# Optimization experiments

Measured on AMD Instinct MI355X. Metric: run time of the kernel, lower is better.

## Reference

```python
import jax, jax.numpy as jnp
import numpy as np

ZERO_EXP = -128.0  # exponent assigned to (near-)zero values, matching torch int8 fill


def _exp_quant_dequant(t):
    """Round-trip through the ExpFloat format.

    exponent = clamp(round(log2(|t|)), -128, 127) for |t| > 1e-38 else -128.
    Dequant is pow(2, exponent) -- note the sign is DISCARDED (faithful to
    ExpFloat.to_tensor, which never applies the stored sign), so the result
    is always positive.
    """
    a = jnp.abs(t)
    mask = a > 1e-38
    # guard log2 input with 1.0 where masked to avoid -inf/nan
    e = jnp.clip(jnp.round(jnp.log2(jnp.where(mask, a, 1.0))), -128.0, 127.0)
    e = jnp.where(mask, e, ZERO_EXP)
    return jnp.exp2(e)


def setup_inputs() -> dict:
    key = jax.random.key(0)
    k1, k2, k3 = jax.random.split(key, 3)
    N, IN, OUT = 8192, 4096, 4096
    x = jax.random.normal(k1, (N, IN), dtype=jnp.float32)
    # kaiming-uniform-ish scale for weight, uniform bias bound 1/sqrt(fan_in)
    bound_w = float(np.sqrt(6.0 / ((1.0 + 5.0) * IN)))
    weight = jax.random.uniform(k2, (OUT, IN), dtype=jnp.float32,
                                minval=-bound_w, maxval=bound_w)
    bound_b = 1.0 / float(np.sqrt(IN))
    bias = jax.random.uniform(k3, (OUT,), dtype=jnp.float32,
                              minval=-bound_b, maxval=bound_b)
    return {"x": x, "weight": weight, "bias": bias}


def reference(x, weight, bias):
    # quantized forward path of ExpFloatLinear (after .quantize()):
    # 1) x and W.T are quantized to power-of-two magnitudes (sign dropped)
    xq = _exp_quant_dequant(x)             # [N, IN]
    wq = _exp_quant_dequant(weight.T)      # [IN, OUT]
    # 2) dense matmul in dequantized domain
    m = jnp.matmul(xq, wq)                 # [N, OUT]
    # 3) matmul result re-quantized (ExpFloat.matmul returns ExpFloat(result))
    mq = _exp_quant_dequant(m)
    # 4) bias dequantized, added, and the sum quantized once more before to_tensor
    bq = _exp_quant_dequant(bias)          # [OUT]
    out = _exp_quant_dequant(mq + bq)      # [N, OUT]
    return out
```

## Files before the change

### kernel.cpp

```cpp
#include <hip/hip_runtime.h>
#include <hip/hip_bf16.h>
#include <stdint.h>

typedef __attribute__((ext_vector_type(8))) short short8;
typedef __attribute__((ext_vector_type(4))) float f32x4;

#define M_ROWS 8192
#define K_DIM  4096
#define N_COLS 4096
#define NT     (K_DIM / 64)
#define NWG    ((M_ROWS / 256) * (N_COLS / 256))
#define WL_CAP (1 << 20)

#define SQRT2_MANT 0x6A09E667F3BCDLL
#define FLAG_MARGIN 3110000000000LL

__device__ __forceinline__ int rlog2_mask(double a) {
    if (!(a > 1e-38)) return -128;
    long long b = __double_as_longlong(a);
    int E = (int)(b >> 52) - 1023;
    long long m = b & 0xFFFFFFFFFFFFFLL;
    int e = E + (int)(m >= SQRT2_MANT);
    return e < -128 ? -128 : (e > 127 ? 127 : e);
}

__device__ __forceinline__ double pow2d(int e) {
    return __longlong_as_double((long long)(e + 1023) << 52);
}

__device__ __forceinline__ unsigned short bf16_pow2(int e) {
    if (e >= -126) return (unsigned short)((e + 127) << 7);
    int sh = 133 + e;
    return (unsigned short)(sh >= 0 ? (1 << sh) : 0);
}

__device__ __forceinline__ int bf16_exp(unsigned short u) {
    int ex = (u >> 7) & 0xFF;
    if (ex) return ex - 127;
    int m = u & 0x7F;
    return m ? (-133 + (31 - __clz(m))) : -1000;
}

__device__ __forceinline__ float finalize_out(int em, int ebj) {
    double s = pow2d(em) + pow2d(ebj);
    return (float)pow2d(rlog2_mask(s));
}

__global__ void quant_kernel(const float* __restrict__ in, unsigned short* __restrict__ outq, int n4) {
    int idx = blockIdx.x * blockDim.x + threadIdx.x;
    int stride = gridDim.x * blockDim.x;
    for (int i = idx; i < n4; i += stride) {
        float4 v = ((const float4*)in)[i];
        ushort4 o;
        o.x = bf16_pow2(rlog2_mask(fabs((double)v.x)));
        o.y = bf16_pow2(rlog2_mask(fabs((double)v.y)));
        o.z = bf16_pow2(rlog2_mask(fabs((double)v.z)));
        o.w = bf16_pow2(rlog2_mask(fabs((double)v.w)));
        ((ushort4*)outq)[i] = o;
    }
}

__global__ void quant_bias_kernel(const float* __restrict__ b, int* __restrict__ eb, int n) {
    int i = blockIdx.x * blockDim.x + threadIdx.x;
    if (i < n) eb[i] = rlog2_mask(fabs((double)b[i]));
}

__device__ __forceinline__ void g2lds16(const unsigned short* g, unsigned short* l) {
    __builtin_amdgcn_global_load_lds(
        (const __attribute__((address_space(1))) unsigned int*)g,
        (__attribute__((address_space(3))) unsigned int*)l, 16, 0, 0);
}

#define LD8(p, off) (*(const short8*)((const char*)(p) + (off)))
#define MFMA16(a, b, c) __builtin_amdgcn_mfma_f32_16x16x32_bf16((a), (b), (c), 0, 0, 0)

__global__ __launch_bounds__(512, 2) void gemm_kernel(
    const unsigned short* __restrict__ xq, const unsigned short* __restrict__ wq,
    const int* __restrict__ eb, float* __restrict__ out,
    int* __restrict__ wl_count, int* __restrict__ wl)
{
    __shared__ unsigned short lds[2][32768];

    const int tid = threadIdx.x;
    const int lane = tid & 63, w = tid >> 6;
    const int wm = w >> 2, wn = w & 3;
    const int l15 = lane & 15, lhi = lane >> 4;

    const int x = blockIdx.x & 7;
    const int j = blockIdx.x >> 3;
    const int bm = (x & 3) * 8 + (j & 7);
    const int bn = (x >> 2) * 8 + ((j >> 3) & 3) + (j >> 5) * 4;
    const int brow = bm * 256, bcol = bn * 256;

    int p0 = tid * 16;
    int lin0 = p0 ^ (((p0 >> 9) & 1) << 5);
    int row0 = (lin0 >> 6) & 127;
    int col0 = (((lin0 >> 13) << 6) | (lin0 & 63)) >> 1;
    int p1 = 8192 + tid * 16;
    int lin1 = p1 ^ (((p1 >> 9) & 1) << 5);
    int row1 = (lin1 >> 6) & 127;
    int col1 = (((lin1 >> 13) << 6) | (lin1 & 63)) >> 1;

    const unsigned short* aS0h0 = xq + (size_t)(brow + row0) * K_DIM + col0;
    const unsigned short* aS1h0 = xq + (size_t)(brow + row1) * K_DIM + col1;
    const unsigned short* aS0h1 = aS0h0 + (size_t)128 * K_DIM;
    const unsigned short* aS1h1 = aS1h0 + (size_t)128 * K_DIM;
    const unsigned short* bS0h0 = wq + (size_t)(bcol + row0) * K_DIM + col0;
    const unsigned short* bS1h0 = wq + (size_t)(bcol + row1) * K_DIM + col1;
    const unsigned short* bS0h1 = bS0h0 + (size_t)128 * K_DIM;
    const unsigned short* bS1h1 = bS1h0 + (size_t)128 * K_DIM;

    const int wofs = w * 512;

#define STAGE_A(b, h, OFFE) do { \
        g2lds16(((h) ? aS0h1 : aS0h0) + (OFFE), &lds[b][(h) * 8192] + wofs); \
        g2lds16(((h) ? aS1h1 : aS1h0) + (OFFE), &lds[b][(h) * 8192 + 4096] + wofs); \
    } while (0)
#define STAGE_B(b, h, OFFE) do { \
        g2lds16(((h) ? bS0h1 : bS0h0) + (OFFE), &lds[b][16384 + (h) * 8192] + wofs); \
        g2lds16(((h) ? bS1h1 : bS1h0) + (OFFE), &lds[b][16384 + (h) * 8192 + 4096] + wofs); \
    } while (0)

    int fsw = l15 * 64 + lhi * 16;
    fsw ^= ((l15 >> 3) & 1) << 5;

    const char* pA_0 = (const char*)&lds[0][wm * 8192] + fsw;
    const char* pA_1 = (const char*)&lds[1][wm * 8192] + fsw;
    const char* pB_0 = (const char*)&lds[0][16384 + (wn >> 1) * 8192 + (wn & 1) * 2048] + fsw;
    const char* pB_1 = (const char*)&lds[1][16384 + (wn >> 1) * 8192 + (wn & 1) * 2048] + fsw;

    f32x4 acc[8][4];
#pragma unroll
    for (int m = 0; m < 8; ++m)
#pragma unroll
        for (int n = 0; n < 4; ++n) acc[m][n] = (f32x4){0.f, 0.f, 0.f, 0.f};

    short8 aF[4][2], b01[2][2], b23[2][2];

#define DS_A4(P, mb) do { \
        aF[0][0] = LD8(P, ((mb) + 0) * 1024); aF[0][1] = LD8(P, ((mb) + 0) * 1024 + 8192); \
        aF[1][0] = LD8(P, ((mb) + 1) * 1024); aF[1][1] = LD8(P, ((mb) + 1) * 1024 + 8192); \
        aF[2][0] = LD8(P, ((mb) + 2) * 1024); aF[2][1] = LD8(P, ((mb) + 2) * 1024 + 8192); \
        aF[3][0] = LD8(P, ((mb) + 3) * 1024); aF[3][1] = LD8(P, ((mb) + 3) * 1024 + 8192); \
    } while (0)
#define DS_B2(P, arr, cb) do { \
        arr[0][0] = LD8(P, ((cb) + 0) * 1024); arr[0][1] = LD8(P, ((cb) + 0) * 1024 + 8192); \
        arr[1][0] = LD8(P, ((cb) + 1) * 1024); arr[1][1] = LD8(P, ((cb) + 1) * 1024 + 8192); \
    } while (0)
#define MFMA_Q(mb, nb, B) do { \
        _Pragma("unroll") \
        for (int m_ = 0; m_ < 4; ++m_) \
        _Pragma("unroll") \
        for (int n_ = 0; n_ < 2; ++n_) { \
            acc[(mb) + m_][(nb) + n_] = MFMA16(aF[m_][0], B[n_][0], acc[(mb) + m_][(nb) + n_]); \
            acc[(mb) + m_][(nb) + n_] = MFMA16(aF[m_][1], B[n_][1], acc[(mb) + m_][(nb) + n_]); \
        } \
    } while (0)

#define BAR()  __builtin_amdgcn_s_barrier()
#define PRIO1() __builtin_amdgcn_s_setprio(1)
#define PRIO0() __builtin_amdgcn_s_setprio(0)

    STAGE_A(0, 0, 0);
    STAGE_A(0, 1, 0);
    STAGE_B(0, 0, 0);
    STAGE_B(0, 1, 0);
    STAGE_B(1, 0, 64);
    STAGE_B(1, 1, 64);
    asm volatile("s_waitcnt vmcnt(4)" ::: "memory");
    BAR();

    for (int tt = 0; tt < NT / 2 - 1; ++tt) {
        DS_B2(pB_0, b01, 0); DS_B2(pB_0, b23, 2);
        DS_A4(pA_0, 0);
        STAGE_A(1, 0, 64); STAGE_A(1, 1, 64);
        PRIO1(); MFMA_Q(0, 0, b01); MFMA_Q(0, 2, b23); PRIO0(); BAR();
        DS_A4(pA_0, 4);
        STAGE_B(0, 0, 128); STAGE_B(0, 1, 128);
        PRIO1(); MFMA_Q(4, 2, b23); MFMA_Q(4, 0, b01); PRIO0();
        asm volatile("s_waitcnt vmcnt(4)" ::: "memory");
        BAR();
        DS_B2(pB_1, b01, 0); DS_B2(pB_1, b23, 2);
        DS_A4(pA_1, 0);
        STAGE_A(0, 0, 128); STAGE_A(0, 1, 128);
        PRIO1(); MFMA_Q(0, 0, b01); MFMA_Q(0, 2, b23); PRIO0(); BAR();
        DS_A4(pA_1, 4);
        STAGE_B(1, 0, 192); STAGE_B(1, 1, 192);
        PRIO1(); MFMA_Q(4, 2, b23); MFMA_Q(4, 0, b01); PRIO0();
        asm volatile("s_waitcnt vmcnt(4)" ::: "memory");
        BAR();

        aS0h0 += 128; aS1h0 += 128; aS0h1 += 128; aS1h1 += 128;
        bS0h0 += 128; bS1h0 += 128; bS0h1 += 128; bS1h1 += 128;
    }

    DS_B2(pB_0, b01, 0); DS_B2(pB_0, b23, 2);
    DS_A4(pA_0, 0);
    STAGE_A(1, 0, 64); STAGE_A(1, 1, 64);
    PRIO1(); MFMA_Q(0, 0, b01); MFMA_Q(0, 2, b23); PRIO0(); BAR();
    DS_A4(pA_0, 4);
    PRIO1(); MFMA_Q(4, 2, b23); MFMA_Q(4, 0, b01); PRIO0();
    asm volatile("s_waitcnt vmcnt(0)" ::: "memory");
    BAR();
    DS_B2(pB_1, b01, 0); DS_B2(pB_1, b23, 2);
    DS_A4(pA_1, 0);
    PRIO1(); MFMA_Q(0, 0, b01); MFMA_Q(0, 2, b23); PRIO0(); BAR();
    DS_A4(pA_1, 4);
    PRIO1(); MFMA_Q(4, 2, b23); MFMA_Q(4, 0, b01); PRIO0();

#pragma unroll
    for (int m = 0; m < 8; ++m) {
        int grow_base = brow + wm * 128 + m * 16 + lhi * 4;
#pragma unroll
        for (int n = 0; n < 4; ++n) {
            int gcol = bcol + wn * 64 + n * 16 + l15;
            int ebj = eb[gcol];
#pragma unroll
            for (int q = 0; q < 4; ++q) {
                float S = acc[m][n][q];
                int grow = grow_base + q;
                double v = (double)S;
                int em; bool flag;
                if (v > 1e-38) {
                    long long bb = __double_as_longlong(v);
                    long long mm = bb & 0xFFFFFFFFFFFFFLL;
                    long long d = mm - SQRT2_MANT;
                    flag = (d < 0 ? -d : d) < FLAG_MARGIN;
                    int e = ((int)(bb >> 52) - 1023) + (int)(mm >= SQRT2_MANT);
                    em = e < -128 ? -128 : (e > 127 ? 127 : e);
                } else { em = -128; flag = true; }
                out[(size_t)grow * N_COLS + gcol] = finalize_out(em, ebj);
                if (flag) {
                    int pos = atomicAdd(wl_count, 1);
                    if (pos < WL_CAP) wl[pos] = grow * N_COLS + gcol;
                }
            }
        }
    }
}

__global__ __launch_bounds__(256) void fixup_kernel(
    const unsigned short* __restrict__ xq, const unsigned short* __restrict__ wq,
    const int* __restrict__ eb, float* __restrict__ out,
    const int* __restrict__ wl_count, const int* __restrict__ wl)
{
    const int nwaves = (gridDim.x * blockDim.x) >> 6;
    const int gw = (blockIdx.x * blockDim.x + threadIdx.x) >> 6;
    const int lane = threadIdx.x & 63;
    int count = *wl_count;
    if (count > WL_CAP) count = WL_CAP;
    for (int it = gw; it < count; it += nwaves) {
        int lin = wl[it];
        int i = lin >> 12;
        int j = lin & 4095;
        const unsigned short* xr = xq + (size_t)i * K_DIM;
        const unsigned short* wr = wq + (size_t)j * K_DIM;
        unsigned long long accu = 0;
        for (int kb = 0; kb < K_DIM / 256; ++kb) {
            int k0 = kb * 256 + lane * 4;
            ushort4 xv = *(const ushort4*)(xr + k0);
            ushort4 wv = *(const ushort4*)(wr + k0);
            int p;
            p = bf16_exp(xv.x) + bf16_exp(wv.x) + 56; if ((unsigned)p <= 62u) accu += 1ULL << p;
            p = bf16_exp(xv.y) + bf16_exp(wv.y) + 56; if ((unsigned)p <= 62u) accu += 1ULL << p;
            p = bf16_exp(xv.z) + bf16_exp(wv.z) + 56; if ((unsigned)p <= 62u) accu += 1ULL << p;
            p = bf16_exp(xv.w) + bf16_exp(wv.w) + 56; if ((unsigned)p <= 62u) accu += 1ULL << p;
        }
#pragma unroll
        for (int off = 32; off; off >>= 1) accu += __shfl_down(accu, off, 64);
        if (lane == 0) {
            double S = (double)accu * 0x1p-56;
            int em = rlog2_mask(S);
            out[lin] = finalize_out(em, eb[j]);
        }
    }
}

extern "C" void kernel_launch(void* const* d_in, const int* in_sizes, int n_in,
                              void* d_out, int out_size, void* d_ws, size_t ws_size,
                              hipStream_t stream) {
    const float* x    = (const float*)d_in[0];
    const float* w    = (const float*)d_in[1];
    const float* bias = (const float*)d_in[2];
    float* out = (float*)d_out;
    char* ws = (char*)d_ws;

    int* wl_count = (int*)ws;
    int* eb       = (int*)(ws + 256);
    unsigned short* xq = (unsigned short*)(ws + 32768);
    unsigned short* wq = (unsigned short*)(ws + 32768 + (size_t)M_ROWS * K_DIM * 2);
    int* wl = (int*)(ws + 32768 + (size_t)M_ROWS * K_DIM * 2 + (size_t)N_COLS * K_DIM * 2);

    hipMemsetAsync(wl_count, 0, 4, stream);
    quant_kernel<<<2048, 256, 0, stream>>>(x, xq, M_ROWS * K_DIM / 4);
    quant_kernel<<<1024, 256, 0, stream>>>(w, wq, N_COLS * K_DIM / 4);
    quant_bias_kernel<<<16, 256, 0, stream>>>(bias, eb, N_COLS);
    gemm_kernel<<<dim3(NWG), 512, 0, stream>>>(xq, wq, eb, out, wl_count, wl);
    fixup_kernel<<<1024, 256, 0, stream>>>(xq, wq, eb, out, wl_count, wl);
}
```

Measured before the change: 290.7 us.

## Make GEMM persistent over two row tiles and fuse quant launches

The GEMM grid is halved from 512 to 256 workgroups. Each workgroup now loops over two 256-row tiles that share the same column block, which removes the partial second wave on a 256-CU device and may improve L2 reuse of the weight tile. The x and w quantization kernels are merged into one launch to save a kernel launch. The tradeoffs are the prologue and epilogue that are now serialized per tile inside each workgroup, and a loss of latency hiding between neighbouring workgroups.

```diff
diff --git a/kernel.cpp b/kernel.cpp
--- a/kernel.cpp
+++ b/kernel.cpp
@@ -9,7 +9,6 @@
 #define K_DIM  4096
 #define N_COLS 4096
 #define NT     (K_DIM / 64)
-#define NWG    ((M_ROWS / 256) * (N_COLS / 256))
 #define WL_CAP (1 << 20)
 
 #define SQRT2_MANT 0x6A09E667F3BCDLL
@@ -46,17 +45,29 @@
     return (float)pow2d(rlog2_mask(s));
 }
 
-__global__ void quant_kernel(const float* __restrict__ in, unsigned short* __restrict__ outq, int n4) {
+__device__ __forceinline__ ushort4 quant4(float4 v) {
+    ushort4 o;
+    o.x = bf16_pow2(rlog2_mask(fabs((double)v.x)));
+    o.y = bf16_pow2(rlog2_mask(fabs((double)v.y)));
+    o.z = bf16_pow2(rlog2_mask(fabs((double)v.z)));
+    o.w = bf16_pow2(rlog2_mask(fabs((double)v.w)));
+    return o;
+}
+
+__global__ void quant_kernel(const float* __restrict__ x, const float* __restrict__ w,
+                             unsigned short* __restrict__ xq, unsigned short* __restrict__ wq,
+                             int nx4, int nw4) {
     int idx = blockIdx.x * blockDim.x + threadIdx.x;
     int stride = gridDim.x * blockDim.x;
-    for (int i = idx; i < n4; i += stride) {
-        float4 v = ((const float4*)in)[i];
-        ushort4 o;
-        o.x = bf16_pow2(rlog2_mask(fabs((double)v.x)));
-        o.y = bf16_pow2(rlog2_mask(fabs((double)v.y)));
-        o.z = bf16_pow2(rlog2_mask(fabs((double)v.z)));
-        o.w = bf16_pow2(rlog2_mask(fabs((double)v.w)));
-        ((ushort4*)outq)[i] = o;
+    int total = nx4 + nw4;
+    for (int i = idx; i < total; i += stride) {
+        if (i < nx4) {
+            float4 v = ((const float4*)x)[i];
+            ((ushort4*)xq)[i] = quant4(v);
+        } else {
+            float4 v = ((const float4*)w)[i - nx4];
+            ((ushort4*)wq)[i - nx4] = quant4(v);
+        }
     }
 }
 
@@ -88,9 +99,9 @@
 
     const int x = blockIdx.x & 7;
     const int j = blockIdx.x >> 3;
-    const int bm = (x & 3) * 8 + (j & 7);
-    const int bn = (x >> 2) * 8 + ((j >> 3) & 3) + (j >> 5) * 4;
-    const int brow = bm * 256, bcol = bn * 256;
+    const int bm0 = (x & 3) * 8 + (j & 3);
+    const int bn  = (x >> 2) * 8 + (j >> 2);
+    const int bcol = bn * 256;
 
     int p0 = tid * 16;
     int lin0 = p0 ^ (((p0 >> 9) & 1) << 5);
@@ -101,26 +112,6 @@
     int row1 = (lin1 >> 6) & 127;
     int col1 = (((lin1 >> 13) << 6) | (lin1 & 63)) >> 1;
 
-    const unsigned short* aS0h0 = xq + (size_t)(brow + row0) * K_DIM + col0;
-    const unsigned short* aS1h0 = xq + (size_t)(brow + row1) * K_DIM + col1;
-    const unsigned short* aS0h1 = aS0h0 + (size_t)128 * K_DIM;
-    const unsigned short* aS1h1 = aS1h0 + (size_t)128 * K_DIM;
-    const unsigned short* bS0h0 = wq + (size_t)(bcol + row0) * K_DIM + col0;
-    const unsigned short* bS1h0 = wq + (size_t)(bcol + row1) * K_DIM + col1;
-    const unsigned short* bS0h1 = bS0h0 + (size_t)128 * K_DIM;
-    const unsigned short* bS1h1 = bS1h0 + (size_t)128 * K_DIM;
-
-    const int wofs = w * 512;
-
-#define STAGE_A(b, h, OFFE) do { \
-        g2lds16(((h) ? aS0h1 : aS0h0) + (OFFE), &lds[b][(h) * 8192] + wofs); \
-        g2lds16(((h) ? aS1h1 : aS1h0) + (OFFE), &lds[b][(h) * 8192 + 4096] + wofs); \
-    } while (0)
-#define STAGE_B(b, h, OFFE) do { \
-        g2lds16(((h) ? bS0h1 : bS0h0) + (OFFE), &lds[b][16384 + (h) * 8192] + wofs); \
-        g2lds16(((h) ? bS1h1 : bS1h0) + (OFFE), &lds[b][16384 + (h) * 8192 + 4096] + wofs); \
-    } while (0)
-
     int fsw = l15 * 64 + lhi * 16;
     fsw ^= ((l15 >> 3) & 1) << 5;
 
@@ -129,14 +120,14 @@
     const char* pB_0 = (const char*)&lds[0][16384 + (wn >> 1) * 8192 + (wn & 1) * 2048] + fsw;
     const char* pB_1 = (const char*)&lds[1][16384 + (wn >> 1) * 8192 + (wn & 1) * 2048] + fsw;
 
-    f32x4 acc[8][4];
-#pragma unroll
-    for (int m = 0; m < 8; ++m)
-#pragma unroll
-        for (int n = 0; n < 4; ++n) acc[m][n] = (f32x4){0.f, 0.f, 0.f, 0.f};
-
-    short8 aF[4][2], b01[2][2], b23[2][2];
-
+#define STAGE_A(b, h, OFFE) do { \
+        g2lds16(((h) ? aS0h1 : aS0h0) + (OFFE), &lds[b][(h) * 8192] + wofs); \
+        g2lds16(((h) ? aS1h1 : aS1h0) + (OFFE), &lds[b][(h) * 8192 + 4096] + wofs); \
+    } while (0)
+#define STAGE_B(b, h, OFFE) do { \
+        g2lds16(((h) ? bS0h1 : bS0h0) + (OFFE), &lds[b][16384 + (h) * 8192] + wofs); \
+        g2lds16(((h) ? bS1h1 : bS1h0) + (OFFE), &lds[b][16384 + (h) * 8192 + 4096] + wofs); \
+    } while (0)
 #define DS_A4(P, mb) do { \
         aF[0][0] = LD8(P, ((mb) + 0) * 1024); aF[0][1] = LD8(P, ((mb) + 0) * 1024 + 8192); \
         aF[1][0] = LD8(P, ((mb) + 1) * 1024); aF[1][1] = LD8(P, ((mb) + 1) * 1024 + 8192); \
@@ -161,78 +152,104 @@
 #define PRIO1() __builtin_amdgcn_s_setprio(1)
 #define PRIO0() __builtin_amdgcn_s_setprio(0)
 
-    STAGE_A(0, 0, 0);
-    STAGE_A(0, 1, 0);
-    STAGE_B(0, 0, 0);
-    STAGE_B(0, 1, 0);
-    STAGE_B(1, 0, 64);
-    STAGE_B(1, 1, 64);
-    asm volatile("s_waitcnt vmcnt(4)" ::: "memory");
-    BAR();
-
-    for (int tt = 0; tt < NT / 2 - 1; ++tt) {
+    const int wofs = w * 512;
+
+    for (int ht = 0; ht < 2; ++ht) {
+        const int bm = bm0 + ht * 4;
+        const int brow = bm * 256;
+
+        const unsigned short* aS0h0 = xq + (size_t)(brow + row0) * K_DIM + col0;
+        const unsigned short* aS1h0 = xq + (size_t)(brow + row1) * K_DIM + col1;
+        const unsigned short* aS0h1 = aS0h0 + (size_t)128 * K_DIM;
+        const unsigned short* aS1h1 = aS1h0 + (size_t)128 * K_DIM;
+        const unsigned short* bS0h0 = wq + (size_t)(bcol + row0) * K_DIM + col0;
+        const unsigned short* bS1h0 = wq + (size_t)(bcol + row1) * K_DIM + col1;
+        const unsigned short* bS0h1 = bS0h0 + (size_t)128 * K_DIM;
+        const unsigned short* bS1h1 = bS1h0 + (size_t)128 * K_DIM;
+
+        f32x4 acc[8][4];
+#pragma unroll
+        for (int m = 0; m < 8; ++m)
+#pragma unroll
+            for (int n = 0; n < 4; ++n) acc[m][n] = (f32x4){0.f, 0.f, 0.f, 0.f};
+
+        short8 aF[4][2], b01[2][2], b23[2][2];
+
+        STAGE_A(0, 0, 0);
+        STAGE_A(0, 1, 0);
+        STAGE_B(0, 0, 0);
+        STAGE_B(0, 1, 0);
+        STAGE_B(1, 0, 64);
+        STAGE_B(1, 1, 64);
+        asm volatile("s_waitcnt vmcnt(4)" ::: "memory");
+        BAR();
+
+        for (int tt = 0; tt < NT / 2 - 1; ++tt) {
+            DS_B2(pB_0, b01, 0); DS_B2(pB_0, b23, 2);
+            DS_A4(pA_0, 0);
+            STAGE_A(1, 0, 64); STAGE_A(1, 1, 64);
+            PRIO1(); MFMA_Q(0, 0, b01); MFMA_Q(0, 2, b23); PRIO0(); BAR();
+            DS_A4(pA_0, 4);
+            STAGE_B(0, 0, 128); STAGE_B(0, 1, 128);
+            PRIO1(); MFMA_Q(4, 2, b23); MFMA_Q(4, 0, b01); PRIO0();
+            asm volatile("s_waitcnt vmcnt(4)" ::: "memory");
+            BAR();
+            DS_B2(pB_1, b01, 0); DS_B2(pB_1, b23, 2);
+            DS_A4(pA_1, 0);
+            STAGE_A(0, 0, 128); STAGE_A(0, 1, 128);
+            PRIO1(); MFMA_Q(0, 0, b01); MFMA_Q(0, 2, b23); PRIO0(); BAR();
+            DS_A4(pA_1, 4);
+            STAGE_B(1, 0, 192); STAGE_B(1, 1, 192);
+            PRIO1(); MFMA_Q(4, 2, b23); MFMA_Q(4, 0, b01); PRIO0();
+            asm volatile("s_waitcnt vmcnt(4)" ::: "memory");
+            BAR();
+
+            aS0h0 += 128; aS1h0 += 128; aS0h1 += 128; aS1h1 += 128;
+            bS0h0 += 128; bS1h0 += 128; bS0h1 += 128; bS1h1 += 128;
+        }
+
         DS_B2(pB_0, b01, 0); DS_B2(pB_0, b23, 2);
         DS_A4(pA_0, 0);
         STAGE_A(1, 0, 64); STAGE_A(1, 1, 64);
         PRIO1(); MFMA_Q(0, 0, b01); MFMA_Q(0, 2, b23); PRIO0(); BAR();
         DS_A4(pA_0, 4);
-        STAGE_B(0, 0, 128); STAGE_B(0, 1, 128);
         PRIO1(); MFMA_Q(4, 2, b23); MFMA_Q(4, 0, b01); PRIO0();
-        asm volatile("s_waitcnt vmcnt(4)" ::: "memory");
+        asm volatile("s_waitcnt vmcnt(0)" ::: "memory");
         BAR();
         DS_B2(pB_1, b01, 0); DS_B2(pB_1, b23, 2);
         DS_A4(pA_1, 0);
-        STAGE_A(0, 0, 128); STAGE_A(0, 1, 128);
         PRIO1(); MFMA_Q(0, 0, b01); MFMA_Q(0, 2, b23); PRIO0(); BAR();
         DS_A4(pA_1, 4);
-        STAGE_B(1, 0, 192); STAGE_B(1, 1, 192);
         PRIO1(); MFMA_Q(4, 2, b23); MFMA_Q(4, 0, b01); PRIO0();
-        asm volatile("s_waitcnt vmcnt(4)" ::: "memory");
+
         BAR();
 
-        aS0h0 += 128; aS1h0 += 128; aS0h1 += 128; aS1h1 += 128;
-        bS0h0 += 128; bS1h0 += 128; bS0h1 += 128; bS1h1 += 128;
-    }
-
-    DS_B2(pB_0, b01, 0); DS_B2(pB_0, b23, 2);
-    DS_A4(pA_0, 0);
-    STAGE_A(1, 0, 64); STAGE_A(1, 1, 64);
-    PRIO1(); MFMA_Q(0, 0, b01); MFMA_Q(0, 2, b23); PRIO0(); BAR();
-    DS_A4(pA_0, 4);
-    PRIO1(); MFMA_Q(4, 2, b23); MFMA_Q(4, 0, b01); PRIO0();
-    asm volatile("s_waitcnt vmcnt(0)" ::: "memory");
-    BAR();
-    DS_B2(pB_1, b01, 0); DS_B2(pB_1, b23, 2);
-    DS_A4(pA_1, 0);
-    PRIO1(); MFMA_Q(0, 0, b01); MFMA_Q(0, 2, b23); PRIO0(); BAR();
-    DS_A4(pA_1, 4);
-    PRIO1(); MFMA_Q(4, 2, b23); MFMA_Q(4, 0, b01); PRIO0();
-
-#pragma unroll
-    for (int m = 0; m < 8; ++m) {
-        int grow_base = brow + wm * 128 + m * 16 + lhi * 4;
-#pragma unroll
-        for (int n = 0; n < 4; ++n) {
-            int gcol = bcol + wn * 64 + n * 16 + l15;
-            int ebj = eb[gcol];
-#pragma unroll
-            for (int q = 0; q < 4; ++q) {
-                float S = acc[m][n][q];
-                int grow = grow_base + q;
-                double v = (double)S;
-                int em; bool flag;
-                if (v > 1e-38) {
-                    long long bb = __double_as_longlong(v);
-                    long long mm = bb & 0xFFFFFFFFFFFFFLL;
-                    long long d = mm - SQRT2_MANT;
-                    flag = (d < 0 ? -d : d) < FLAG_MARGIN;
-                    int e = ((int)(bb >> 52) - 1023) + (int)(mm >= SQRT2_MANT);
-                    em = e < -128 ? -128 : (e > 127 ? 127 : e);
-                } else { em = -128; flag = true; }
-                out[(size_t)grow * N_COLS + gcol] = finalize_out(em, ebj);
-                if (flag) {
-                    int pos = atomicAdd(wl_count, 1);
-                    if (pos < WL_CAP) wl[pos] = grow * N_COLS + gcol;
+#pragma unroll
+        for (int m = 0; m < 8; ++m) {
+            int grow_base = brow + wm * 128 + m * 16 + lhi * 4;
+#pragma unroll
+            for (int n = 0; n < 4; ++n) {
+                int gcol = bcol + wn * 64 + n * 16 + l15;
+                int ebj = eb[gcol];
+#pragma unroll
+                for (int q = 0; q < 4; ++q) {
+                    float S = acc[m][n][q];
+                    int grow = grow_base + q;
+                    double v = (double)S;
+                    int em; bool flag;
+                    if (v > 1e-38) {
+                        long long bb = __double_as_longlong(v);
+                        long long mm = bb & 0xFFFFFFFFFFFFFLL;
+                        long long d = mm - SQRT2_MANT;
+                        flag = (d < 0 ? -d : d) < FLAG_MARGIN;
+                        int e = ((int)(bb >> 52) - 1023) + (int)(mm >= SQRT2_MANT);
+                        em = e < -128 ? -128 : (e > 127 ? 127 : e);
+                    } else { em = -128; flag = true; }
+                    out[(size_t)grow * N_COLS + gcol] = finalize_out(em, ebj);
+                    if (flag) {
+                        int pos = atomicAdd(wl_count, 1);
+                        if (pos < WL_CAP) wl[pos] = grow * N_COLS + gcol;
+                    }
                 }
             }
         }
@@ -292,9 +309,9 @@
     int* wl = (int*)(ws + 32768 + (size_t)M_ROWS * K_DIM * 2 + (size_t)N_COLS * K_DIM * 2);
 
     hipMemsetAsync(wl_count, 0, 4, stream);
-    quant_kernel<<<2048, 256, 0, stream>>>(x, xq, M_ROWS * K_DIM / 4);
-    quant_kernel<<<1024, 256, 0, stream>>>(w, wq, N_COLS * K_DIM / 4);
+    quant_kernel<<<3072, 256, 0, stream>>>(x, w, xq, wq,
+                                           M_ROWS * K_DIM / 4, N_COLS * K_DIM / 4);
     quant_bias_kernel<<<16, 256, 0, stream>>>(bias, eb, N_COLS);
-    gemm_kernel<<<dim3(NWG), 512, 0, stream>>>(xq, wq, eb, out, wl_count, wl);
+    gemm_kernel<<<dim3(256), 512, 0, stream>>>(xq, wq, eb, out, wl_count, wl);
     fixup_kernel<<<1024, 256, 0, stream>>>(xq, wq, eb, out, wl_count, wl);
 }
```

Result: faster. 278.4 us (-4.2%).
